# Performance work log

Hardware: AMD Instinct MI355X
Metric: run time of the kernel (lower is better)

The kernel has to match this reference:

```python
import jax, jax.numpy as jnp
import numpy as np
from jax import lax

DIM = 128
HEADS = 4
B, H, W = 8, 128, 128


def conv1x1(x, w, b):
    # x: [B,C,H,W], w: [O,I,1,1]
    y = lax.conv_general_dilated(x, w, (1, 1), 'VALID',
                                 dimension_numbers=('NCHW', 'OIHW', 'NCHW'))
    return y + b[None, :, None, None]


def dwconv3x3(x, w, b):
    # depthwise: w: [C,1,3,3], groups=C
    C = x.shape[1]
    y = lax.conv_general_dilated(x, w, (1, 1), ((1, 1), (1, 1)),
                                 dimension_numbers=('NCHW', 'OIHW', 'NCHW'),
                                 feature_group_count=C)
    return y + b[None, :, None, None]


def setup_inputs() -> dict:
    key = jax.random.key(0)
    ks = jax.random.split(key, 7)
    s = 0.02
    return {
        'x': jax.random.normal(ks[0], (B, DIM, H, W), jnp.float32),
        'qkv_w': jax.random.normal(ks[1], (3 * DIM, DIM, 1, 1), jnp.float32) * s,
        'qkv_b': jnp.zeros((3 * DIM,), jnp.float32),
        'dw_w': jax.random.normal(ks[2], (3 * DIM, 1, 3, 3), jnp.float32) * s,
        'dw_b': jnp.zeros((3 * DIM,), jnp.float32),
        'proj_w': jax.random.normal(ks[3], (DIM, DIM, 1, 1), jnp.float32) * s,
        'proj_b': jnp.zeros((DIM,), jnp.float32),
        'temperature': jnp.ones((HEADS, 1, 1, 1), jnp.float32),
    }


def reference(x, qkv_w, qkv_b, dw_w, dw_b, proj_w, proj_b, temperature):
    b, C, h, w = x.shape
    heads = temperature.shape[0]
    c = C // heads

    qkv = dwconv3x3(conv1x1(x, qkv_w, qkv_b), dw_w, dw_b)
    q, k, v = jnp.split(qkv, 3, axis=1)

    # b (head c) h w -> b head c h w
    q = q.reshape(b, heads, c, h, w)
    k = k.reshape(b, heads, c, h, w)
    v = v.reshape(b, heads, c, h, w)

    # L2-normalize along H (axis=-2), matching torch F.normalize eps=1e-12
    eps = 1e-12
    q = q / jnp.maximum(jnp.linalg.norm(q, axis=-2, keepdims=True), eps)
    k = k / jnp.maximum(jnp.linalg.norm(k, axis=-2, keepdims=True), eps)

    # attn[b,n,c,j,k] = sum_i q[b,n,c,i,j] * k_[b,n,c,i,k]  -> [b,head,c,W,W]
    attn = jnp.einsum('bncij,bncik->bncjk', q, k) * temperature
    attn = jax.nn.softmax(attn, axis=-2)

    # out[b,n,c,i,k] = sum_j v[b,n,c,i,j] * attn[b,n,c,j,k]
    out = jnp.einsum('bncij,bncjk->bncik', v, attn)
    out = out.reshape(b, C, h, w)
    return conv1x1(out, proj_w, proj_b)
```

## Files before the change

kernel.cpp:

```cpp
#include <hip/hip_runtime.h>

typedef unsigned short u16;
typedef unsigned int   u32;

typedef short bf16x8 __attribute__((ext_vector_type(8)));
typedef float f32x4  __attribute__((ext_vector_type(4)));

__device__ __forceinline__ float bf2f(u16 u) { return __uint_as_float(((u32)u) << 16); }
__device__ __forceinline__ u16 f2bf(float f) {
    u32 u = __float_as_uint(f);
    return (u16)((u + 0x7fffu + ((u >> 16) & 1u)) >> 16);
}

#define MFMA16(a, b, c) __builtin_amdgcn_mfma_f32_16x16x32_bf16(a, b, c, 0, 0, 0)

__global__ __launch_bounds__(256, 4) void k_xpose(const float* __restrict__ x,
                                                  u16* __restrict__ xT) {
    __shared__ u16 Xs[128 * 128];
    const int ptile = blockIdx.x, b = blockIdx.y;
    const int t = threadIdx.x;
    const float* xb = x + (((size_t)b) << 21) + ptile * 128;
#pragma unroll
    for (int i = 0; i < 16; ++i) {
        int idx = i * 256 + t;
        int ci = idx >> 5, pq = idx & 31;
        float4 v = *(const float4*)(xb + (((size_t)ci) << 14) + pq * 4);
        u32 lo = (u32)f2bf(v.x) | ((u32)f2bf(v.y) << 16);
        u32 hi = (u32)f2bf(v.z) | ((u32)f2bf(v.w) << 16);
        uint2 pk; pk.x = lo; pk.y = hi;
        int cq = ci >> 3;
        *(uint2*)(&Xs[ci * 128 + ((pq ^ cq) << 2)]) = pk;
    }
    __syncthreads();
    u16* ob = xT + (((size_t)b) << 21) + ((size_t)(ptile * 128)) * 128;
#pragma unroll
    for (int j = 0; j < 8; ++j) {
        int p = j * 16 + (t >> 4), cq = t & 15;
        u16 tmp[8];
#pragma unroll
        for (int c = 0; c < 8; ++c) {
            int ci = cq * 8 + c;
            tmp[c] = Xs[ci * 128 + (((p >> 2) ^ cq) << 2) + (p & 3)];
        }
        *(uint4*)(&ob[(size_t)p * 128 + cq * 8]) = *(const uint4*)tmp;
    }
}

__global__ __launch_bounds__(512, 6) void k_qkv(const u16* __restrict__ xT,
                                                const float* __restrict__ w,
                                                const float* __restrict__ bias,
                                                u16* __restrict__ out1) {
    extern __shared__ char smem[];
    u16* Bt = (u16*)smem;
    u16* Cs = Bt + 2048 * 8;
    const int h = blockIdx.x, cg = blockIdx.y, b = blockIdx.z;
    const int t = threadIdx.x;

    const u16* xb = xT + (((size_t)b) << 21) + ((size_t)(h * 128)) * 128;
#pragma unroll
    for (int i = 0; i < 4; ++i) {
        int slot = i * 512 + t;
        int p = slot >> 4, g = slot & 15;
        int gg = g ^ (p & 15);
        uint4 v = *(const uint4*)(&xb[p * 128 + gg * 8]);
        *(uint4*)(&Bt[slot * 8]) = v;
    }

    const int wave = t >> 6, lane = t & 63, m16 = lane & 15, quad = lane >> 4;
    bf16x8 afr[4];
    {
        const float* wp0 = w + (size_t)(cg * 128 + wave * 16 + m16) * 128 + quad * 8;
#pragma unroll
        for (int kk = 0; kk < 4; ++kk) {
            float4 w0 = *(const float4*)(wp0 + kk * 32);
            float4 w1 = *(const float4*)(wp0 + kk * 32 + 4);
            bf16x8 a;
            a[0] = (short)f2bf(w0.x); a[1] = (short)f2bf(w0.y);
            a[2] = (short)f2bf(w0.z); a[3] = (short)f2bf(w0.w);
            a[4] = (short)f2bf(w1.x); a[5] = (short)f2bf(w1.y);
            a[6] = (short)f2bf(w1.z); a[7] = (short)f2bf(w1.w);
            afr[kk] = a;
        }
    }
    __syncthreads();

    f32x4 acc[8] = {};
#pragma unroll
    for (int kk = 0; kk < 4; ++kk) {
        const int g = kk * 4 + quad;
#pragma unroll
        for (int nt = 0; nt < 8; ++nt) {
            int p = nt * 16 + m16;
            bf16x8 bf = *(const bf16x8*)(&Bt[p * 128 + ((g ^ (p & 15)) << 3)]);
            acc[nt] = MFMA16(afr[kk], bf, acc[nt]);
        }
    }

    float bv[4];
#pragma unroll
    for (int r = 0; r < 4; ++r) bv[r] = bias[cg * 128 + wave * 16 + quad * 4 + r];

    u16* ob = out1 + (((size_t)(b * 384 + cg * 128)) << 14) + (h << 7);

    if (wave < 4) {
#pragma unroll
        for (int nt = 0; nt < 8; ++nt) {
            int p = nt * 16 + m16;
#pragma unroll
            for (int r = 0; r < 4; ++r)
                Cs[(wave * 16 + quad * 4 + r) * 136 + p] = f2bf(acc[nt][r] + bv[r]);
        }
    }
    __syncthreads();
#pragma unroll
    for (int it = 0; it < 2; ++it) {
        int idx = it * 512 + t;
        int co = idx >> 4, cp = idx & 15;
        *(uint4*)(&ob[((size_t)co << 14) + cp * 8]) = *(const uint4*)(&Cs[co * 136 + cp * 8]);
    }
    __syncthreads();

    if (wave >= 4) {
#pragma unroll
        for (int nt = 0; nt < 8; ++nt) {
            int p = nt * 16 + m16;
#pragma unroll
            for (int r = 0; r < 4; ++r)
                Cs[((wave - 4) * 16 + quad * 4 + r) * 136 + p] = f2bf(acc[nt][r] + bv[r]);
        }
    }
    __syncthreads();
    u16* ob2 = ob + ((size_t)64 << 14);
#pragma unroll
    for (int it = 0; it < 2; ++it) {
        int idx = it * 512 + t;
        int co = idx >> 4, cp = idx & 15;
        *(uint4*)(&ob2[((size_t)co << 14) + cp * 8]) = *(const uint4*)(&Cs[co * 136 + cp * 8]);
    }
}

__global__ __launch_bounds__(256, 4) void k_dw(const u16* __restrict__ in,
                                               const float* __restrict__ w,
                                               const float* __restrict__ bias,
                                               u16* __restrict__ out) {
    __shared__ u16 tile[34 * 144];
    const int htile = blockIdx.x;
    const int ch = blockIdx.y;
    const int b = blockIdx.z;
    const int t = threadIdx.x;
    const u16* base = in + (((size_t)(b * 384 + ch)) << 14);

    if (t < 68) {
        int r = t >> 1, side = t & 1;
        uint4 z = {0, 0, 0, 0};
        *(uint4*)(&tile[r * 144 + side * 136]) = z;
    }
    for (int it = 0; it < 3; ++it) {
        int idx = it * 256 + t;
        if (idx < 544) {
            int r = idx >> 4, cq = idx & 15;
            int y = htile * 32 - 1 + r;
            uint4 v = {0, 0, 0, 0};
            if (y >= 0 && y <= 127) v = *(const uint4*)(base + (y << 7) + cq * 8);
            *(uint4*)(&tile[r * 144 + 8 + cq * 8]) = v;
        }
    }
    float wg[9];
#pragma unroll
    for (int i = 0; i < 9; ++i) wg[i] = w[ch * 9 + i];
    const float bv = bias[ch];
    __syncthreads();

    const int r = t >> 4, cp = t & 15, c0 = cp * 8;
    u16* ob = out + (((size_t)(b * 384 + ch)) << 14) + ((htile * 32) << 7) + c0;
#pragma unroll
    for (int half = 0; half < 2; ++half) {
        const int ro = r + half * 16;
        float acc[8];
#pragma unroll
        for (int c = 0; c < 8; ++c) acc[c] = bv;
#pragma unroll
        for (int dy = 0; dy < 3; ++dy) {
            const u16* row = &tile[(ro + dy) * 144 + 8 + c0];
            float v[10];
            v[0] = bf2f(row[-1]);
            uint4 m = *(const uint4*)row;
            v[1] = bf2f((u16)(m.x & 0xffff)); v[2] = bf2f((u16)(m.x >> 16));
            v[3] = bf2f((u16)(m.y & 0xffff)); v[4] = bf2f((u16)(m.y >> 16));
            v[5] = bf2f((u16)(m.z & 0xffff)); v[6] = bf2f((u16)(m.z >> 16));
            v[7] = bf2f((u16)(m.w & 0xffff)); v[8] = bf2f((u16)(m.w >> 16));
            v[9] = bf2f(row[8]);
#pragma unroll
            for (int dx = 0; dx < 3; ++dx) {
                const float wv = wg[dy * 3 + dx];
#pragma unroll
                for (int c = 0; c < 8; ++c) acc[c] += wv * v[c + dx];
            }
        }
        u32 pk[4];
#pragma unroll
        for (int c2 = 0; c2 < 4; ++c2) {
            u32 lo = f2bf(acc[2 * c2]), hi = f2bf(acc[2 * c2 + 1]);
            pk[c2] = lo | (hi << 16);
        }
        *(uint4*)(ob + (ro << 7)) = *(uint4*)pk;
    }
}

__global__ __launch_bounds__(512, 4) void k_attn(const u16* __restrict__ qkv,
                                                 const float* __restrict__ temp,
                                                 u16* __restrict__ outp) {
    extern __shared__ char smem[];
    u16* Qt = (u16*)smem;
    u16* Kt = Qt + 16384;
    u16* Sg = Qt + 32768;
    float* ps = (float*)(smem + 74752);
    float* rq = (float*)(smem + 76800);
    float* rk = (float*)(smem + 77312);
    u16* Pt = Qt;
    u16* Osh = Kt;

    const int ch = blockIdx.x, b = blockIdx.y;
    const int head = ch >> 5;
    const int t = threadIdx.x;
    const size_t qoff = ((size_t)(b * 384 + ch)) << 14;
    const size_t koff = ((size_t)(b * 384 + 128 + ch)) << 14;
    const size_t voff = ((size_t)(b * 384 + 256 + ch)) << 14;

    const int wave = t >> 6, lane = t & 63, m16 = lane & 15, quad = lane >> 4;

    bf16x8 vfr[4];
    {
        const u16* vrow = qkv + voff + (size_t)(wave * 16 + m16) * 128 + quad * 8;
#pragma unroll
        for (int kk = 0; kk < 4; ++kk)
            vfr[kk] = *(const bf16x8*)(vrow + kk * 32);
    }

    const int ldr = t >> 4, ldj8 = t & 15;
    const size_t ldsrc = (ldr < 16 ? qoff + (size_t)ldr * 128
                                   : koff + (size_t)(ldr - 16) * 128) + ldj8 * 8;
    const int gmat = t >> 8, gig = (t >> 7) & 1, gj = t & 127;
    const u16* gcol = &Sg[(gmat * 16 + gig * 8) * 144 + gj];
    u16* gdstbase = (gmat ? Kt : Qt) + gj * 128;
    float ssq = 0.f;
#pragma unroll
    for (int p = 0; p < 8; ++p) {
        *(uint4*)(&Sg[ldr * 144 + ldj8 * 8]) = *(const uint4*)(&qkv[ldsrc + (size_t)p * 2048]);
        __syncthreads();
        u16 tmp[8];
#pragma unroll
        for (int c = 0; c < 8; ++c) {
            u16 v = gcol[c * 144];
            tmp[c] = v;
            float f = bf2f(v);
            ssq += f * f;
        }
        int g = p * 2 + gig;
        *(uint4*)(gdstbase + ((g ^ (gj & 15)) << 3)) = *(const uint4*)tmp;
        __syncthreads();
    }
    ps[(gmat * 2 + gig) * 128 + gj] = ssq;
    __syncthreads();
    if (t < 256) {
        int mat = t >> 7, j = t & 127;
        float s = ps[(mat * 2) * 128 + j] + ps[(mat * 2 + 1) * 128 + j];
        float r = 1.0f / fmaxf(sqrtf(s), 1e-12f);
        if (mat == 0) rq[j] = r; else rk[j] = r;
    }
    __syncthreads();

    f32x4 S[8] = {};
#pragma unroll
    for (int kk = 0; kk < 4; ++kk) {
        const int sw = ((kk * 4 + quad) ^ m16) << 3;
        bf16x8 bf = *(const bf16x8*)(&Kt[(wave * 16 + m16) * 128 + sw]);
#pragma unroll
        for (int jt = 0; jt < 8; ++jt) {
            bf16x8 af = *(const bf16x8*)(&Qt[(jt * 16 + m16) * 128 + sw]);
            S[jt] = MFMA16(af, bf, S[jt]);
        }
    }

    const float sc = temp[head] * rk[wave * 16 + m16];
    float vals[8][4];
    float vmax = -1e30f;
#pragma unroll
    for (int jt = 0; jt < 8; ++jt)
#pragma unroll
        for (int r = 0; r < 4; ++r) {
            float v = S[jt][r] * (rq[jt * 16 + quad * 4 + r] * sc);
            vals[jt][r] = v;
            vmax = fmaxf(vmax, v);
        }
    vmax = fmaxf(vmax, __shfl_xor(vmax, 16));
    vmax = fmaxf(vmax, __shfl_xor(vmax, 32));
    float sum = 0.f;
#pragma unroll
    for (int jt = 0; jt < 8; ++jt)
#pragma unroll
        for (int r = 0; r < 4; ++r) {
            float e = __expf(vals[jt][r] - vmax);
            vals[jt][r] = e;
            sum += e;
        }
    sum += __shfl_xor(sum, 16);
    sum += __shfl_xor(sum, 32);
    const float inv = 1.0f / sum;

    __syncthreads();

    {
        const int k = wave * 16 + m16;
        u16* prow = Pt + k * 128;
#pragma unroll
        for (int jt = 0; jt < 8; ++jt)
#pragma unroll
            for (int pr = 0; pr < 2; ++pr) {
                int j0 = jt * 16 + quad * 4 + pr * 2;
                u32 pk = (u32)f2bf(vals[jt][pr * 2] * inv) |
                         ((u32)f2bf(vals[jt][pr * 2 + 1] * inv) << 16);
                *(u32*)(prow + (((j0 >> 3) ^ (k & 15)) << 3) + (j0 & 7)) = pk;
            }
    }
    __syncthreads();

    f32x4 O[8] = {};
#pragma unroll
    for (int kk = 0; kk < 4; ++kk) {
        const int sw = ((kk * 4 + quad) ^ m16) << 3;
#pragma unroll
        for (int nt = 0; nt < 8; ++nt) {
            bf16x8 bf = *(const bf16x8*)(&Pt[(nt * 16 + m16) * 128 + sw]);
            O[nt] = MFMA16(vfr[kk], bf, O[nt]);
        }
    }

#pragma unroll
    for (int nt = 0; nt < 8; ++nt) {
        int k = nt * 16 + m16;
#pragma unroll
        for (int r = 0; r < 4; ++r) {
            int i = wave * 16 + quad * 4 + r;
            Osh[i * 128 + (((k >> 3) ^ (i & 15)) << 3) + (k & 7)] = f2bf(O[nt][r]);
        }
    }
    __syncthreads();

    u16* ob = outp + (((size_t)(b * 128 + ch)) << 14);
#pragma unroll
    for (int it = 0; it < 4; ++it) {
        int idx = it * 512 + t;
        int row = idx >> 4, gk = idx & 15;
        uint4 v = *(const uint4*)(&Osh[row * 128 + ((gk ^ (row & 15)) << 3)]);
        *(uint4*)(&ob[(row << 7) + gk * 8]) = v;
    }
}

__global__ __launch_bounds__(512, 6) void k_proj(const u16* __restrict__ ain,
                                                 const float* __restrict__ w,
                                                 const float* __restrict__ bias,
                                                 float* __restrict__ outp) {
    extern __shared__ char smem[];
    u16* Bt = (u16*)smem;
    u16* Sg = Bt + 16384;
    const int h = blockIdx.x, b = blockIdx.y;
    const int t = threadIdx.x;

    const int ldr = t >> 4, ldj8 = t & 15;
    const int gig = t >> 7, gp = t & 127;
    const u16* gcol = &Sg[(gig * 8) * 144 + gp];
    u16* gdst = Bt + gp * 128;
#pragma unroll
    for (int ph = 0; ph < 4; ++ph) {
        int ch = ph * 32 + ldr;
        *(uint4*)(&Sg[ldr * 144 + ldj8 * 8]) =
            *(const uint4*)(&ain[(((size_t)(b * 128 + ch)) << 14) + (h << 7) + ldj8 * 8]);
        __syncthreads();
        u16 tmp[8];
#pragma unroll
        for (int c = 0; c < 8; ++c) tmp[c] = gcol[c * 144];
        int g = ph * 4 + gig;
        *(uint4*)(gdst + ((g ^ (gp & 15)) << 3)) = *(const uint4*)tmp;
        __syncthreads();
    }

    const int wave = t >> 6, lane = t & 63, m16 = lane & 15, quad = lane >> 4;
    bf16x8 afr[4];
    {
        const float* wp0 = w + (size_t)(wave * 16 + m16) * 128 + quad * 8;
#pragma unroll
        for (int kk = 0; kk < 4; ++kk) {
            float4 w0 = *(const float4*)(wp0 + kk * 32);
            float4 w1 = *(const float4*)(wp0 + kk * 32 + 4);
            bf16x8 a;
            a[0] = (short)f2bf(w0.x); a[1] = (short)f2bf(w0.y);
            a[2] = (short)f2bf(w0.z); a[3] = (short)f2bf(w0.w);
            a[4] = (short)f2bf(w1.x); a[5] = (short)f2bf(w1.y);
            a[6] = (short)f2bf(w1.z); a[7] = (short)f2bf(w1.w);
            afr[kk] = a;
        }
    }

    f32x4 acc[8] = {};
#pragma unroll
    for (int kk = 0; kk < 4; ++kk) {
        const int g = kk * 4 + quad;
#pragma unroll
        for (int nt = 0; nt < 8; ++nt) {
            int p = nt * 16 + m16;
            bf16x8 bf = *(const bf16x8*)(&Bt[p * 128 + ((g ^ (p & 15)) << 3)]);
            acc[nt] = MFMA16(afr[kk], bf, acc[nt]);
        }
    }

    float bv[4];
#pragma unroll
    for (int r = 0; r < 4; ++r) bv[r] = bias[wave * 16 + quad * 4 + r];
    float* ob = outp + (((size_t)(b * 128)) << 14) + (h << 7);
#pragma unroll
    for (int nt = 0; nt < 8; ++nt) {
        int p = nt * 16 + m16;
#pragma unroll
        for (int r = 0; r < 4; ++r) {
            int co = wave * 16 + quad * 4 + r;
            ob[((size_t)co << 14) + p] = acc[nt][r] + bv[r];
        }
    }
}

extern "C" void kernel_launch(void* const* d_in, const int* in_sizes, int n_in,
                              void* d_out, int out_size, void* d_ws, size_t ws_size,
                              hipStream_t stream) {
    const float* x      = (const float*)d_in[0];
    const float* qkv_w  = (const float*)d_in[1];
    const float* qkv_b  = (const float*)d_in[2];
    const float* dw_w   = (const float*)d_in[3];
    const float* dw_b   = (const float*)d_in[4];
    const float* proj_w = (const float*)d_in[5];
    const float* proj_b = (const float*)d_in[6];
    const float* temp   = (const float*)d_in[7];
    float* out = (float*)d_out;

    u16* buf1 = (u16*)d_ws;
    u16* buf2 = buf1 + (size_t)8 * 384 * 16384;

    hipFuncSetAttribute((const void*)k_qkv,  hipFuncAttributeMaxDynamicSharedMemorySize, 50176);
    hipFuncSetAttribute((const void*)k_attn, hipFuncAttributeMaxDynamicSharedMemorySize, 77824);
    hipFuncSetAttribute((const void*)k_proj, hipFuncAttributeMaxDynamicSharedMemorySize, 41984);

    k_xpose<<<dim3(128, 8), 256, 0, stream>>>(x, buf2);
    k_qkv<<<dim3(128, 3, 8), 512, 50176, stream>>>(buf2, qkv_w, qkv_b, buf1);
    k_dw<<<dim3(4, 384, 8), 256, 0, stream>>>(buf1, dw_w, dw_b, buf2);
    k_attn<<<dim3(128, 8), 512, 77824, stream>>>(buf2, temp, buf1);
    k_proj<<<dim3(128, 8), 512, 41984, stream>>>(buf1, proj_w, proj_b, out);
}
```

Measured before the change: 253.6 us.

## Fuse depthwise 3x3 conv into attention kernel, drop separate k_dw pass

Removes the standalone depthwise-conv kernel and computes the 3x3 depthwise conv inside the attention kernel: V is staged in shared memory with halo and convolved into MFMA fragments, while Q/K row slabs with halos are loaded per step and convolved column-wise before normalization and transposition. This eliminates a full write and read of the 384-channel intermediate tensor and one kernel launch. In exchange, each attention block redoes halo loads and extra ALU work and uses slightly more shared memory, which may affect occupancy.

```diff
diff --git a/kernel.cpp b/kernel.cpp
--- a/kernel.cpp
+++ b/kernel.cpp
@@ -139,84 +139,19 @@
     }
 }
 
-__global__ __launch_bounds__(256, 4) void k_dw(const u16* __restrict__ in,
-                                               const float* __restrict__ w,
-                                               const float* __restrict__ bias,
-                                               u16* __restrict__ out) {
-    __shared__ u16 tile[34 * 144];
-    const int htile = blockIdx.x;
-    const int ch = blockIdx.y;
-    const int b = blockIdx.z;
-    const int t = threadIdx.x;
-    const u16* base = in + (((size_t)(b * 384 + ch)) << 14);
-
-    if (t < 68) {
-        int r = t >> 1, side = t & 1;
-        uint4 z = {0, 0, 0, 0};
-        *(uint4*)(&tile[r * 144 + side * 136]) = z;
-    }
-    for (int it = 0; it < 3; ++it) {
-        int idx = it * 256 + t;
-        if (idx < 544) {
-            int r = idx >> 4, cq = idx & 15;
-            int y = htile * 32 - 1 + r;
-            uint4 v = {0, 0, 0, 0};
-            if (y >= 0 && y <= 127) v = *(const uint4*)(base + (y << 7) + cq * 8);
-            *(uint4*)(&tile[r * 144 + 8 + cq * 8]) = v;
-        }
-    }
-    float wg[9];
-#pragma unroll
-    for (int i = 0; i < 9; ++i) wg[i] = w[ch * 9 + i];
-    const float bv = bias[ch];
-    __syncthreads();
-
-    const int r = t >> 4, cp = t & 15, c0 = cp * 8;
-    u16* ob = out + (((size_t)(b * 384 + ch)) << 14) + ((htile * 32) << 7) + c0;
-#pragma unroll
-    for (int half = 0; half < 2; ++half) {
-        const int ro = r + half * 16;
-        float acc[8];
-#pragma unroll
-        for (int c = 0; c < 8; ++c) acc[c] = bv;
-#pragma unroll
-        for (int dy = 0; dy < 3; ++dy) {
-            const u16* row = &tile[(ro + dy) * 144 + 8 + c0];
-            float v[10];
-            v[0] = bf2f(row[-1]);
-            uint4 m = *(const uint4*)row;
-            v[1] = bf2f((u16)(m.x & 0xffff)); v[2] = bf2f((u16)(m.x >> 16));
-            v[3] = bf2f((u16)(m.y & 0xffff)); v[4] = bf2f((u16)(m.y >> 16));
-            v[5] = bf2f((u16)(m.z & 0xffff)); v[6] = bf2f((u16)(m.z >> 16));
-            v[7] = bf2f((u16)(m.w & 0xffff)); v[8] = bf2f((u16)(m.w >> 16));
-            v[9] = bf2f(row[8]);
-#pragma unroll
-            for (int dx = 0; dx < 3; ++dx) {
-                const float wv = wg[dy * 3 + dx];
-#pragma unroll
-                for (int c = 0; c < 8; ++c) acc[c] += wv * v[c + dx];
-            }
-        }
-        u32 pk[4];
-#pragma unroll
-        for (int c2 = 0; c2 < 4; ++c2) {
-            u32 lo = f2bf(acc[2 * c2]), hi = f2bf(acc[2 * c2 + 1]);
-            pk[c2] = lo | (hi << 16);
-        }
-        *(uint4*)(ob + (ro << 7)) = *(uint4*)pk;
-    }
-}
-
 __global__ __launch_bounds__(512, 4) void k_attn(const u16* __restrict__ qkv,
+                                                 const float* __restrict__ dww,
+                                                 const float* __restrict__ dwb,
                                                  const float* __restrict__ temp,
                                                  u16* __restrict__ outp) {
     extern __shared__ char smem[];
     u16* Qt = (u16*)smem;
     u16* Kt = Qt + 16384;
-    u16* Sg = Qt + 32768;
-    float* ps = (float*)(smem + 74752);
-    float* rq = (float*)(smem + 76800);
-    float* rk = (float*)(smem + 77312);
+    u16* Vr = (u16*)smem;
+    u16* Sg2 = Qt + 32768;
+    float* ps = (float*)(smem + 75904);
+    float* rq = (float*)(smem + 77952);
+    float* rk = (float*)(smem + 78464);
     u16* Pt = Qt;
     u16* Osh = Kt;
 
@@ -224,42 +159,133 @@
     const int head = ch >> 5;
     const int t = threadIdx.x;
     const size_t qoff = ((size_t)(b * 384 + ch)) << 14;
-    const size_t koff = ((size_t)(b * 384 + 128 + ch)) << 14;
-    const size_t voff = ((size_t)(b * 384 + 256 + ch)) << 14;
+    const size_t koff = qoff + ((size_t)128 << 14);
+    const size_t voff = qoff + ((size_t)256 << 14);
 
     const int wave = t >> 6, lane = t & 63, m16 = lane & 15, quad = lane >> 4;
+
+#pragma unroll
+    for (int i = 0; i < 4; ++i) {
+        int idx = i * 512 + t;
+        int r = idx >> 4, c16 = idx & 15;
+        *(uint4*)(&Vr[r * 144 + 8 + c16 * 8]) =
+            *(const uint4*)(&qkv[voff + ((size_t)r << 7) + c16 * 8]);
+    }
+    if (t < 256) {
+        int r = t >> 1, side = t & 1;
+        uint4 z = {0, 0, 0, 0};
+        *(uint4*)(&Vr[r * 144 + side * 136]) = z;
+    } else if (t < 328) {
+        int i = t - 256;
+        int row = i >> 1, side = i & 1;
+        uint4 z = {0, 0, 0, 0};
+        *(uint4*)(&Sg2[row * 144 + side * 136]) = z;
+    }
+    __syncthreads();
 
     bf16x8 vfr[4];
     {
-        const u16* vrow = qkv + voff + (size_t)(wave * 16 + m16) * 128 + quad * 8;
-#pragma unroll
-        for (int kk = 0; kk < 4; ++kk)
-            vfr[kk] = *(const bf16x8*)(vrow + kk * 32);
-    }
-
-    const int ldr = t >> 4, ldj8 = t & 15;
-    const size_t ldsrc = (ldr < 16 ? qoff + (size_t)ldr * 128
-                                   : koff + (size_t)(ldr - 16) * 128) + ldj8 * 8;
+        float wv9[9];
+        const float* wp = dww + (size_t)(256 + ch) * 9;
+#pragma unroll
+        for (int i = 0; i < 9; ++i) wv9[i] = wp[i];
+        const float bvv = dwb[256 + ch];
+        const int r = wave * 16 + m16;
+#pragma unroll
+        for (int kk = 0; kk < 4; ++kk) {
+            const int c0 = quad * 8 + kk * 32;
+            float acc[8];
+#pragma unroll
+            for (int c = 0; c < 8; ++c) acc[c] = bvv;
+#pragma unroll
+            for (int dy = 0; dy < 3; ++dy) {
+                int rr = r + dy - 1;
+                float v[10];
+                if ((unsigned)rr < 128u) {
+                    const u16* row = &Vr[rr * 144 + 8 + c0];
+                    v[0] = bf2f(row[-1]);
+                    uint4 m = *(const uint4*)row;
+                    v[1] = bf2f((u16)(m.x & 0xffff)); v[2] = bf2f((u16)(m.x >> 16));
+                    v[3] = bf2f((u16)(m.y & 0xffff)); v[4] = bf2f((u16)(m.y >> 16));
+                    v[5] = bf2f((u16)(m.z & 0xffff)); v[6] = bf2f((u16)(m.z >> 16));
+                    v[7] = bf2f((u16)(m.w & 0xffff)); v[8] = bf2f((u16)(m.w >> 16));
+                    v[9] = bf2f(row[8]);
+                } else {
+#pragma unroll
+                    for (int i = 0; i < 10; ++i) v[i] = 0.f;
+                }
+#pragma unroll
+                for (int dx = 0; dx < 3; ++dx) {
+                    const float wv = wv9[dy * 3 + dx];
+#pragma unroll
+                    for (int c = 0; c < 8; ++c) acc[c] += wv * v[c + dx];
+                }
+            }
+            bf16x8 a;
+#pragma unroll
+            for (int c = 0; c < 8; ++c) a[c] = (short)f2bf(acc[c]);
+            vfr[kk] = a;
+        }
+    }
+    __syncthreads();
+
     const int gmat = t >> 8, gig = (t >> 7) & 1, gj = t & 127;
-    const u16* gcol = &Sg[(gmat * 16 + gig * 8) * 144 + gj];
     u16* gdstbase = (gmat ? Kt : Qt) + gj * 128;
+    float wg9[9];
+    {
+        const float* wp = dww + (size_t)((gmat ? 128 : 0) + ch) * 9;
+#pragma unroll
+        for (int i = 0; i < 9; ++i) wg9[i] = wp[i];
+    }
+    const float gb = dwb[(gmat ? 128 : 0) + ch];
+    const size_t moff = gmat ? koff : qoff;
     float ssq = 0.f;
-#pragma unroll
+
     for (int p = 0; p < 8; ++p) {
-        *(uint4*)(&Sg[ldr * 144 + ldj8 * 8]) = *(const uint4*)(&qkv[ldsrc + (size_t)p * 2048]);
+#pragma unroll
+        for (int s0 = 0; s0 < 2; ++s0) {
+            int s = s0 * 512 + t;
+            if (s < 576) {
+                int m = (s >= 288) ? 1 : 0;
+                int within = s - m * 288;
+                int lr = within >> 4, c16 = within & 15;
+                int hh = p * 16 - 1 + lr;
+                uint4 v = {0, 0, 0, 0};
+                if ((unsigned)hh < 128u)
+                    v = *(const uint4*)(&qkv[(m ? koff : qoff) + ((size_t)hh << 7) + c16 * 8]);
+                *(uint4*)(&Sg2[(m * 18 + lr) * 144 + 8 + c16 * 8]) = v;
+            }
+        }
         __syncthreads();
+
+        const u16* colp = &Sg2[(gmat * 18 + gig * 8) * 144 + 8 + gj];
+        float cm[10], cc[10], cp_[10];
+#pragma unroll
+        for (int lr = 0; lr < 10; ++lr) {
+            const u16* rp = colp + lr * 144;
+            cm[lr] = bf2f(rp[-1]);
+            cc[lr] = bf2f(rp[0]);
+            cp_[lr] = bf2f(rp[1]);
+        }
         u16 tmp[8];
 #pragma unroll
         for (int c = 0; c < 8; ++c) {
-            u16 v = gcol[c * 144];
-            tmp[c] = v;
-            float f = bf2f(v);
+            float acc = gb;
+#pragma unroll
+            for (int dy = 0; dy < 3; ++dy)
+                acc += wg9[dy * 3 + 0] * cm[c + dy] + wg9[dy * 3 + 1] * cc[c + dy] +
+                       wg9[dy * 3 + 2] * cp_[c + dy];
+            u16 uv = f2bf(acc);
+            tmp[c] = uv;
+            float f = bf2f(uv);
             ssq += f * f;
         }
         int g = p * 2 + gig;
         *(uint4*)(gdstbase + ((g ^ (gj & 15)) << 3)) = *(const uint4*)tmp;
         __syncthreads();
     }
+    (void)moff;
+
     ps[(gmat * 2 + gig) * 128 + gj] = ssq;
     __syncthreads();
     if (t < 256) {
@@ -446,12 +472,11 @@
     u16* buf2 = buf1 + (size_t)8 * 384 * 16384;
 
     hipFuncSetAttribute((const void*)k_qkv,  hipFuncAttributeMaxDynamicSharedMemorySize, 50176);
-    hipFuncSetAttribute((const void*)k_attn, hipFuncAttributeMaxDynamicSharedMemorySize, 77824);
+    hipFuncSetAttribute((const void*)k_attn, hipFuncAttributeMaxDynamicSharedMemorySize, 78976);
     hipFuncSetAttribute((const void*)k_proj, hipFuncAttributeMaxDynamicSharedMemorySize, 41984);
 
     k_xpose<<<dim3(128, 8), 256, 0, stream>>>(x, buf2);
     k_qkv<<<dim3(128, 3, 8), 512, 50176, stream>>>(buf2, qkv_w, qkv_b, buf1);
-    k_dw<<<dim3(4, 384, 8), 256, 0, stream>>>(buf1, dw_w, dw_b, buf2);
-    k_attn<<<dim3(128, 8), 512, 77824, stream>>>(buf2, temp, buf1);
-    k_proj<<<dim3(128, 8), 512, 41984, stream>>>(buf1, proj_w, proj_b, out);
-}
+    k_attn<<<dim3(128, 8), 512, 78976, stream>>>(buf1, dw_w, dw_b, temp, buf2);
+    k_proj<<<dim3(128, 8), 512, 41984, stream>>>(buf2, proj_w, proj_b, out);
+}
```

After: 442.7 us. 1.75x slower.
